# Performance work log

Hardware: AMD Instinct MI355X
Metric: run time of the kernel (lower is better)

The kernel has to match this reference:

```python
import jax, jax.numpy as jnp
import numpy as np

L, B, T, D, H, A, F, V, BIAS_DIM, E = 6, 16, 512, 512, 8, 64, 2048, 10000, 4, 200000
LN_EPS = 1e-3  # keras LayerNormalization default


def positional_encoding(d, max_len):
    pos = np.arange(max_len, dtype=np.float32)[:, None]
    i = np.arange(d, dtype=np.float32)[None, :]
    angle = pos / np.power(10000.0, (2.0 * np.floor(i / 2.0)) / d)
    pe = np.where((np.arange(d) % 2) == 0, np.sin(angle), np.cos(angle))
    return jnp.asarray(pe, jnp.float32)


def layer_norm(x, g, b):
    mu = jnp.mean(x, -1, keepdims=True)
    var = jnp.mean(jnp.square(x - mu), -1, keepdims=True)
    return (x - mu) * jax.lax.rsqrt(var + LN_EPS) * g + b


def attention(x, masks, bias_idx, Wq, Wk, Wv, Wo, be, bs):
    q = jnp.einsum('btd,dha->btha', x, Wq)
    k = jnp.einsum('btd,dha->btha', x, Wk)
    v = jnp.einsum('btd,dha->btha', x, Wv)
    alpha = jnp.einsum('bkha,bqha->bhqk', k, q)
    # sparse edge bias: scalar per edge = bias_embs[type] @ bias_scalar
    ev = (be[bias_idx[:, 0]] @ bs)[:, 0]                      # [E]
    dense = jnp.zeros((x.shape[0], x.shape[1], x.shape[1]), x.dtype)
    dense = dense.at[bias_idx[:, 1], bias_idx[:, 2], bias_idx[:, 3]].add(ev)  # scatter_nd semantics (add)
    ksum = jnp.sum(k, -1)                                     # [B,T,H]
    alpha = alpha + jnp.einsum('bqk,bkh->bhqk', dense, ksum)
    alpha = alpha * jax.lax.rsqrt(jnp.float32(A))
    alpha = alpha * masks + (1.0 - jnp.ceil(masks)) * jnp.finfo(jnp.float32).min
    alpha = jax.nn.softmax(alpha, -1)
    ctx = jnp.einsum('bhqk,bkha->bqha', alpha, v)
    return jnp.einsum('btha,had->btd', ctx, Wo)


def setup_inputs() -> dict:
    key = jax.random.key(0)
    ks = jax.random.split(key, 24)
    tokens = jax.random.randint(ks[0], (B, T), 0, V, dtype=jnp.int32)
    masks = jnp.ones((B, 1, T, T), jnp.float32)
    ab = jnp.stack([
        jax.random.randint(ks[1], (E,), 0, BIAS_DIM, dtype=jnp.int32),
        jax.random.randint(ks[2], (E,), 0, B, dtype=jnp.int32),
        jax.random.randint(ks[3], (E,), 0, T, dtype=jnp.int32),
        jax.random.randint(ks[4], (E,), 0, T, dtype=jnp.int32)], axis=1)
    s = 0.03
    return {
        'tokens': tokens, 'masks': masks, 'attention_bias': ab,
        'embed': jax.random.normal(ks[5], (V, D)) * (D ** -0.5),
        'Wq': jax.random.normal(ks[6], (L, D, H, A)) * s,
        'Wk': jax.random.normal(ks[7], (L, D, H, A)) * s,
        'Wv': jax.random.normal(ks[8], (L, D, H, A)) * s,
        'Wo': jax.random.normal(ks[9], (L, H, A, D)) * s,
        'be': jax.random.normal(ks[10], (L, BIAS_DIM, A)) * s,
        'bs': jax.random.normal(ks[11], (L, A, 1)) * s,
        'ln_g': jnp.ones((L, 2, D)), 'ln_b': jnp.zeros((L, 2, D)),
        'ff1_w': jax.random.normal(ks[12], (L, D, F)) * s,
        'ff1_b': jnp.zeros((L, F)),
        'ff2_w': jax.random.normal(ks[13], (L, F, D)) * s,
        'ff2_b': jnp.zeros((L, D)),
        'lnout_g': jnp.ones((D,)), 'lnout_b': jnp.zeros((D,)),
    }


def reference(tokens, masks, attention_bias, embed, Wq, Wk, Wv, Wo, be, bs,
              ln_g, ln_b, ff1_w, ff1_b, ff2_w, ff2_b, lnout_g, lnout_b):
    pos_enc = positional_encoding(D, 5000)
    x = embed[tokens] * jnp.sqrt(jnp.float32(D)) + pos_enc[:T]
    for l in range(L):
        h = layer_norm(x, ln_g[l, 0], ln_b[l, 0])
        x = x + attention(h, masks, attention_bias, Wq[l], Wk[l], Wv[l], Wo[l], be[l], bs[l])
        h = layer_norm(x, ln_g[l, 1], ln_b[l, 1])
        x = x + jax.nn.relu(h @ ff1_w[l] + ff1_b[l]) @ ff2_w[l] + ff2_b[l]
    return layer_norm(x, lnout_g, lnout_b)
```

## Files before the change

kernel.cpp:

```cpp
#include <hip/hip_runtime.h>
#include <hip/hip_bf16.h>

#define LNUM 6
#define BB 16
#define TT 512
#define DD 512
#define HH 8
#define AA 64
#define FFD 2048
#define EE 200000
#define BIASDIM 4
#define ATT_NEG (-3.402823466e38f)

typedef __bf16 bf16_t;
typedef __attribute__((ext_vector_type(8))) __bf16 bf16x8;
typedef __attribute__((ext_vector_type(4))) float f32x4;

typedef __attribute__((address_space(3))) void lds_void;
typedef const __attribute__((address_space(1))) void glb_void;

__device__ __forceinline__ void async_load16(const bf16_t* g, bf16_t* l) {
    __builtin_amdgcn_global_load_lds((glb_void*)g, (lds_void*)l, 16, 0, 0);
}

__global__ __launch_bounds__(256) void embed_pe_kernel(
    const int* __restrict__ tokens, const float* __restrict__ embed,
    float* __restrict__ x)
{
    int idx = blockIdx.x * 256 + threadIdx.x;
    int d  = idx & (DD - 1);
    int bt = idx >> 9;
    int t  = bt & (TT - 1);
    int tok = tokens[bt];
    float e = embed[(long long)tok * DD + d] * 22.62741699796952f;
    float p = (float)(2 * (d >> 1)) * (1.0f / (float)DD);
    float denom = exp2f(p * 13.287712379549449f);
    float angle = (float)t / denom;
    float pe = (d & 1) ? cosf(angle) : sinf(angle);
    x[idx] = e + pe;
}

template <typename TO>
__global__ __launch_bounds__(256) void ln_kernel(
    const float* __restrict__ x, TO* __restrict__ y,
    const float* __restrict__ g, const float* __restrict__ b)
{
    long long row = blockIdx.x;
    const float* xr = x + row * DD;
    int tid = threadIdx.x;
    float v0 = xr[tid], v1 = xr[tid + 256];
    float s = v0 + v1, sq = v0 * v0 + v1 * v1;
#pragma unroll
    for (int o = 32; o > 0; o >>= 1) {
        s  += __shfl_down(s, o);
        sq += __shfl_down(sq, o);
    }
    __shared__ float ss[4], sq4[4];
    if ((tid & 63) == 0) { ss[tid >> 6] = s; sq4[tid >> 6] = sq; }
    __syncthreads();
    float st  = ss[0] + ss[1] + ss[2] + ss[3];
    float sqt = sq4[0] + sq4[1] + sq4[2] + sq4[3];
    float mean = st * (1.0f / DD);
    float var  = sqt * (1.0f / DD) - mean * mean;
    float inv  = rsqrtf(var + 1e-3f);
    y[row * DD + tid]       = (TO)((v0 - mean) * inv * g[tid]       + b[tid]);
    y[row * DD + tid + 256] = (TO)((v1 - mean) * inv * g[tid + 256] + b[tid + 256]);
}

template <typename TO, int S>
__global__ __launch_bounds__(256) void reduce_ln_kernel(
    float* __restrict__ x, const float* __restrict__ P,
    TO* __restrict__ y, const float* __restrict__ g, const float* __restrict__ b)
{
    const long long NXc = (long long)BB * TT * DD;
    long long row = blockIdx.x;
    int tid = threadIdx.x;
    long long i0 = row * DD + tid;
    float v0 = x[i0], v1 = x[i0 + 256];
#pragma unroll
    for (int s = 0; s < S; s++) {
        v0 += P[(long long)s * NXc + i0];
        v1 += P[(long long)s * NXc + i0 + 256];
    }
    x[i0] = v0; x[i0 + 256] = v1;
    float s2 = v0 + v1, sq = v0 * v0 + v1 * v1;
#pragma unroll
    for (int o = 32; o > 0; o >>= 1) {
        s2 += __shfl_down(s2, o);
        sq += __shfl_down(sq, o);
    }
    __shared__ float ss[4], sq4[4];
    if ((tid & 63) == 0) { ss[tid >> 6] = s2; sq4[tid >> 6] = sq; }
    __syncthreads();
    float st  = ss[0] + ss[1] + ss[2] + ss[3];
    float sqt = sq4[0] + sq4[1] + sq4[2] + sq4[3];
    float mean = st * (1.0f / DD);
    float var  = sqt * (1.0f / DD) - mean * mean;
    float inv  = rsqrtf(var + 1e-3f);
    y[i0]       = (TO)((v0 - mean) * inv * g[tid]       + b[tid]);
    y[i0 + 256] = (TO)((v1 - mean) * inv * g[tid + 256] + b[tid + 256]);
}

__global__ __launch_bounds__(256) void ksum_kernel(
    const bf16_t* __restrict__ k, float* __restrict__ ks)
{
    int idx = blockIdx.x * 256 + threadIdx.x;
    long long base = (long long)idx * AA;
    float s = 0.f;
#pragma unroll
    for (int a = 0; a < AA; a++) s += (float)k[base + a];
    ks[idx] = s;
}

__global__ __launch_bounds__(256) void bias_scatter_kernel(
    const int* __restrict__ ab, const float* __restrict__ be,
    const float* __restrict__ bs, float* __restrict__ dense)
{
    __shared__ float ev[BIASDIM];
    int tid = threadIdx.x;
    if (tid < BIASDIM) {
        float s = 0.f;
        for (int a = 0; a < AA; a++) s += be[tid * AA + a] * bs[a];
        ev[tid] = s;
    }
    __syncthreads();
    int e = blockIdx.x * 256 + tid;
    if (e < EE) {
        int ty = ab[e * 4 + 0];
        int b  = ab[e * 4 + 1];
        int q  = ab[e * 4 + 2];
        int kk = ab[e * 4 + 3];
        unsafeAtomicAdd(&dense[((long long)b * TT + q) * TT + kk], ev[ty]);
    }
}

__global__ __launch_bounds__(256) void wconv_kernel(
    const float* __restrict__ in, bf16_t* __restrict__ out, int R, int Cc)
{
    __shared__ bf16_t tile[64][65];
    int c0 = blockIdx.x * 64, r0 = blockIdx.y * 64;
    int tid = threadIdx.x;
#pragma unroll
    for (int i = 0; i < 16; i++) {
        int idx = tid + i * 256; int r = idx >> 6, c = idx & 63;
        tile[c][r] = (bf16_t)in[(long long)(r0 + r) * Cc + c0 + c];
    }
    __syncthreads();
#pragma unroll
    for (int i = 0; i < 16; i++) {
        int idx = tid + i * 256; int rr = idx >> 6, cc = idx & 63;
        out[(long long)(c0 + rr) * R + r0 + cc] = tile[rr][cc];
    }
}

struct Ptr4 { const float* p[4]; };

__global__ __launch_bounds__(256) void wconv4_kernel(Ptr4 srcs, bf16_t* __restrict__ out)
{
    __shared__ bf16_t tile[64][65];
    int z = blockIdx.z;
    const float* in = srcs.p[z];
    bf16_t* o = out + (long long)z * DD * DD;
    int c0 = blockIdx.x * 64, r0 = blockIdx.y * 64;
    int tid = threadIdx.x;
#pragma unroll
    for (int i = 0; i < 16; i++) {
        int idx = tid + i * 256; int r = idx >> 6, c = idx & 63;
        tile[c][r] = (bf16_t)in[(long long)(r0 + r) * DD + c0 + c];
    }
    __syncthreads();
#pragma unroll
    for (int i = 0; i < 16; i++) {
        int idx = tid + i * 256; int rr = idx >> 6, cc = idx & 63;
        o[(long long)(c0 + rr) * DD + r0 + cc] = tile[rr][cc];
    }
}

__global__ __launch_bounds__(256) void vtrans_kernel(
    const bf16_t* __restrict__ v, bf16_t* __restrict__ vT)
{
    __shared__ bf16_t tile[64][65];
    int bh = blockIdx.y; int b = bh >> 3, h = bh & 7;
    int t0 = blockIdx.x * 64;
    int tid = threadIdx.x;
#pragma unroll
    for (int i = 0; i < 16; i++) {
        int idx = tid + i * 256; int r = idx >> 6, c = idx & 63;
        tile[c][r] = v[((long long)(b * TT + t0 + r) * HH + h) * AA + c];
    }
    __syncthreads();
#pragma unroll
    for (int i = 0; i < 16; i++) {
        int idx = tid + i * 256; int a = idx >> 6, t2 = idx & 63;
        vT[(((long long)b * HH + h) * AA + a) * TT + t0 + t2] = tile[a][t2];
    }
}

__global__ __launch_bounds__(256) void fused_attn_kernel(
    const bf16_t* __restrict__ qg, const bf16_t* __restrict__ kg,
    const bf16_t* __restrict__ vT, const float* __restrict__ dense,
    const float* __restrict__ ksum, const float* __restrict__ masks,
    bf16_t* __restrict__ ctx)
{
    __shared__ __align__(16) bf16_t Ks[64 * 64];
    __shared__ __align__(16) bf16_t Vs[64 * 64];
    __shared__ __align__(16) bf16_t Plds[4 * 16 * 88];

    int tid = threadIdx.x;
    int wave = tid >> 6, lane = tid & 63;
    int row16 = lane & 15, quad = lane >> 4;
    int bh = blockIdx.y; int b = bh >> 3, h = bh & 7;
    int qw = blockIdx.x * 64 + wave * 16;

    bf16x8 qf[2];
    {
        const bf16_t* qp = qg + (((long long)b * TT + qw + row16) * HH + h) * AA + quad * 8;
        qf[0] = *(const bf16x8*)(qp);
        qf[1] = *(const bf16x8*)(qp + 32);
    }

    f32x4 o[4] = {};
    float m_r[4], l_r[4];
#pragma unroll
    for (int r = 0; r < 4; r++) { m_r[r] = -3.0e38f; l_r[r] = 0.f; }

    bf16_t* Pw = Plds + wave * 16 * 88;
    const float* dbase = dense + (long long)b * TT * TT;
    const float* mbase = masks + (long long)b * TT * TT;

    for (int kt = 0; kt < 8; kt++) {
        int t0 = kt * 64;
#pragma unroll
        for (int p = tid; p < 512; p += 256) {
            int r = p >> 3, s = p & 7, c = s ^ (r & 7);
            async_load16(kg + (((long long)b * TT + t0 + r) * HH + h) * AA + c * 8,
                         Ks + p * 8);
        }
#pragma unroll
        for (int p = tid; p < 512; p += 256) {
            int r = p >> 3, s = p & 7, c = s ^ (r & 7);
            async_load16(vT + ((long long)bh * AA + r) * TT + t0 + c * 8,
                         Vs + p * 8);
        }
        __syncthreads();

        f32x4 s4[4] = {};
#pragma unroll
        for (int n = 0; n < 4; n++) {
            int row = n * 16 + row16;
            int sw = row & 7;
            bf16x8 kf0 = *(const bf16x8*)(Ks + row * 64 + ((quad ^ sw) * 8));
            bf16x8 kf1 = *(const bf16x8*)(Ks + row * 64 + (((quad + 4) ^ sw) * 8));
            s4[n] = __builtin_amdgcn_mfma_f32_16x16x32_bf16(qf[0], kf0, s4[n], 0, 0, 0);
            s4[n] = __builtin_amdgcn_mfma_f32_16x16x32_bf16(qf[1], kf1, s4[n], 0, 0, 0);
        }

        float val[4][4];
#pragma unroll
        for (int n = 0; n < 4; n++) {
            int ktok = t0 + n * 16 + row16;
            float ksv = ksum[((long long)b * TT + ktok) * HH + h];
#pragma unroll
            for (int r = 0; r < 4; r++) {
                int qgl = qw + quad * 4 + r;
                float d  = dbase[(long long)qgl * TT + ktok];
                float mk = mbase[(long long)qgl * TT + ktok];
                float vv = 0.125f * fmaf(d, ksv, s4[n][r]);
                val[n][r] = vv * mk + (1.0f - ceilf(mk)) * ATT_NEG;
            }
        }

        float scl[4];
#pragma unroll
        for (int r = 0; r < 4; r++) {
            float mx = fmaxf(fmaxf(val[0][r], val[1][r]), fmaxf(val[2][r], val[3][r]));
#pragma unroll
            for (int off = 1; off < 16; off <<= 1) mx = fmaxf(mx, __shfl_xor(mx, off));
            float mnew = fmaxf(m_r[r], mx);
            float sc = __expf(m_r[r] - mnew);
            float ps = 0.f;
#pragma unroll
            for (int n = 0; n < 4; n++) {
                float p = __expf(val[n][r] - mnew);
                val[n][r] = p;
                ps += p;
            }
#pragma unroll
            for (int off = 1; off < 16; off <<= 1) ps += __shfl_xor(ps, off);
            l_r[r] = l_r[r] * sc + ps;
            m_r[r] = mnew;
            scl[r] = sc;
        }
#pragma unroll
        for (int j = 0; j < 4; j++)
#pragma unroll
            for (int r = 0; r < 4; r++) o[j][r] *= scl[r];

#pragma unroll
        for (int n = 0; n < 4; n++)
#pragma unroll
            for (int r = 0; r < 4; r++)
                Pw[(quad * 4 + r) * 88 + n * 16 + row16] = (bf16_t)val[n][r];
        asm volatile("s_waitcnt lgkmcnt(0)" ::: "memory");

        bf16x8 pa0 = *(const bf16x8*)(Pw + row16 * 88 + quad * 8);
        bf16x8 pa1 = *(const bf16x8*)(Pw + row16 * 88 + 32 + quad * 8);
#pragma unroll
        for (int j = 0; j < 4; j++) {
            int row = j * 16 + row16;
            int sw = row & 7;
            bf16x8 vb0 = *(const bf16x8*)(Vs + row * 64 + ((quad ^ sw) * 8));
            bf16x8 vb1 = *(const bf16x8*)(Vs + row * 64 + (((quad + 4) ^ sw) * 8));
            o[j] = __builtin_amdgcn_mfma_f32_16x16x32_bf16(pa0, vb0, o[j], 0, 0, 0);
            o[j] = __builtin_amdgcn_mfma_f32_16x16x32_bf16(pa1, vb1, o[j], 0, 0, 0);
        }
        __syncthreads();
    }

#pragma unroll
    for (int r = 0; r < 4; r++) {
        float invl = 1.0f / l_r[r];
        int qgl = qw + quad * 4 + r;
        bf16_t* cp = ctx + (((long long)b * TT + qgl) * HH + h) * AA;
#pragma unroll
        for (int j = 0; j < 4; j++)
            cp[j * 16 + row16] = (bf16_t)(o[j][r] * invl);
    }
}

#define PSTAGE(kc0, slot)                                                     \
    {                                                                         \
        bf16_t* At = sm + (slot) * 16384;                                     \
        bf16_t* Bt = At + 8192;                                               \
        _Pragma("unroll")                                                     \
        for (int i = 0; i < 4; i++) {                                         \
            int qq = tid + i * 256;                                           \
            int r = qq >> 3, ck = qq & 7;                                     \
            int cc = (kc0) + ((ck ^ (r & 7)) * 8);                            \
            async_load16(Ag + (long long)(m0 + r) * lda + cc, At + qq * 8);   \
            async_load16(Bg + (long long)(n0 + r) * ldb + cc, Bt + qq * 8);   \
        }                                                                     \
    }

#define PLOAD()                                                               \
    _Pragma("unroll")                                                         \
    for (int mf = 0; mf < 4; mf++) {                                          \
        int ra = wm * 64 + mf * 16 + row16;                                   \
        _Pragma("unroll")                                                     \
        for (int ks2 = 0; ks2 < 2; ks2++)                                     \
            a8[mf][ks2] = *(const bf16x8*)(Ac + ra * 64 +                     \
                              (((ks2 * 4 + quad) ^ (ra & 7)) * 8));           \
    }                                                                         \
    _Pragma("unroll")                                                         \
    for (int nf = 0; nf < 4; nf++) {                                          \
        int rb = wn * 64 + nf * 16 + row16;                                   \
        _Pragma("unroll")                                                     \
        for (int ks2 = 0; ks2 < 2; ks2++)                                     \
            b8[nf][ks2] = *(const bf16x8*)(Bc + rb * 64 +                     \
                              (((ks2 * 4 + quad) ^ (rb & 7)) * 8));           \
    }

#define PMM()                                                                 \
    _Pragma("unroll")                                                         \
    for (int mf = 0; mf < 4; mf++)                                            \
        _Pragma("unroll")                                                     \
        for (int nf = 0; nf < 4; nf++)                                        \
            _Pragma("unroll")                                                 \
            for (int ks2 = 0; ks2 < 2; ks2++)                                 \
                acc[mf][nf] = __builtin_amdgcn_mfma_f32_16x16x32_bf16(        \
                    a8[mf][ks2], b8[nf][ks2], acc[mf][nf], 0, 0, 0);

#define PIPE_BODY(KBEG, NT)                                                   \
    PSTAGE((KBEG), 0);                                                        \
    int c = 0;                                                                \
    for (int t = 0; t < (NT); ++t, c ^= 1) {                                  \
        if (t + 1 < (NT)) {                                                   \
            PSTAGE((KBEG) + (t + 1) * 64, c ^ 1);                             \
            asm volatile("s_waitcnt vmcnt(8)" ::: "memory");                  \
        } else {                                                              \
            asm volatile("s_waitcnt vmcnt(0)" ::: "memory");                  \
        }                                                                     \
        __builtin_amdgcn_sched_barrier(0);                                    \
        __builtin_amdgcn_s_barrier();                                         \
        __builtin_amdgcn_sched_barrier(0);                                    \
        const bf16_t* Ac = sm + c * 16384;                                    \
        const bf16_t* Bc = Ac + 8192;                                         \
        bf16x8 a8[4][2], b8[4][2];                                            \
        PLOAD();                                                              \
        asm volatile("s_waitcnt lgkmcnt(0)" ::: "memory");                    \
        __builtin_amdgcn_sched_barrier(0);                                    \
        __builtin_amdgcn_s_barrier();                                         \
        __builtin_amdgcn_sched_barrier(0);                                    \
        __builtin_amdgcn_s_setprio(1);                                        \
        PMM();                                                                \
        __builtin_amdgcn_s_setprio(0);                                        \
    }

template <typename TC, int ACCUM, int RELU>
__global__ __launch_bounds__(256, 2) void gemm_pipe(
    const bf16_t* __restrict__ Ag, const bf16_t* __restrict__ Bg, TC* __restrict__ Cg,
    int K, int lda, int ldb, int ldc,
    long long sAz, long long sBz, long long sCz,
    const float* __restrict__ bias)
{
    extern __shared__ __align__(16) bf16_t sm[];
    int z = blockIdx.z;
    Ag += z * sAz; Bg += z * sBz; Cg += z * sCz;

    int tid = threadIdx.x;
    int wave = tid >> 6, lane = tid & 63;
    int wm = wave >> 1, wn = wave & 1;
    int row16 = lane & 15, quad = lane >> 4;
    int m0 = blockIdx.x * 128, n0 = blockIdx.y * 128;

    f32x4 acc[4][4] = {};
    int nt = K >> 6;
    PIPE_BODY(0, nt);

#pragma unroll
    for (int mf = 0; mf < 4; mf++) {
#pragma unroll
        for (int nf = 0; nf < 4; nf++) {
#pragma unroll
            for (int r = 0; r < 4; r++) {
                int m = m0 + wm * 64 + mf * 16 + quad * 4 + r;
                int n = n0 + wn * 64 + nf * 16 + row16;
                float vv = acc[mf][nf][r];
                if (bias) vv += bias[n];
                if (ACCUM) vv += (float)Cg[(long long)m * ldc + n];
                if (RELU) vv = fmaxf(vv, 0.f);
                Cg[(long long)m * ldc + n] = (TC)vv;
            }
        }
    }
}

template <int SPLIT>
__global__ __launch_bounds__(256, 2) void gemm_pipe_splitk(
    const bf16_t* __restrict__ Ag, const bf16_t* __restrict__ Bg,
    float* __restrict__ Cg, float* __restrict__ Pg,
    int K, int lda, int ldb, int ldc, const float* __restrict__ bias)
{
    extern __shared__ __align__(16) bf16_t sm[];
    int z = blockIdx.z;
    int kbeg = z * (K / SPLIT);

    int tid = threadIdx.x;
    int wave = tid >> 6, lane = tid & 63;
    int wm = wave >> 1, wn = wave & 1;
    int row16 = lane & 15, quad = lane >> 4;
    int m0 = blockIdx.x * 128, n0 = blockIdx.y * 128;

    f32x4 acc[4][4] = {};
    int nt = (K / SPLIT) >> 6;
    PIPE_BODY(kbeg, nt);

    const long long NXc = (long long)BB * TT * DD;
#pragma unroll
    for (int mf = 0; mf < 4; mf++) {
#pragma unroll
        for (int nf = 0; nf < 4; nf++) {
#pragma unroll
            for (int r = 0; r < 4; r++) {
                int m = m0 + wm * 64 + mf * 16 + quad * 4 + r;
                int n = n0 + wn * 64 + nf * 16 + row16;
                float vv = acc[mf][nf][r];
                long long ci = (long long)m * ldc + n;
                if (z == 0) {
                    if (bias) vv += bias[n];
                    Cg[ci] = Cg[ci] + vv;
                } else {
                    Pg[(long long)(z - 1) * NXc + ci] = vv;
                }
            }
        }
    }
}

extern "C" void kernel_launch(void* const* d_in, const int* in_sizes, int n_in,
                              void* d_out, int out_size, void* d_ws, size_t ws_size,
                              hipStream_t stream)
{
    const int*   tokens = (const int*)d_in[0];
    const float* masks  = (const float*)d_in[1];
    const int*   ab     = (const int*)d_in[2];
    const float* embed  = (const float*)d_in[3];
    const float* Wq     = (const float*)d_in[4];
    const float* Wk     = (const float*)d_in[5];
    const float* Wv     = (const float*)d_in[6];
    const float* Wo     = (const float*)d_in[7];
    const float* be     = (const float*)d_in[8];
    const float* bs     = (const float*)d_in[9];
    const float* ln_g   = (const float*)d_in[10];
    const float* ln_b   = (const float*)d_in[11];
    const float* ff1w   = (const float*)d_in[12];
    const float* ff1b   = (const float*)d_in[13];
    const float* ff2w   = (const float*)d_in[14];
    const float* ff2b   = (const float*)d_in[15];
    const float* lng    = (const float*)d_in[16];
    const float* lnb    = (const float*)d_in[17];
    float* out = (float*)d_out;

    const long long NX = (long long)BB * TT * DD;
    float* x     = (float*)d_ws;
    float* ks    = x + NX;
    bf16_t* h_bf = (bf16_t*)(ks + (long long)BB * TT * HH);
    float* dense = (float*)(h_bf + NX);
    bf16_t* q    = (bf16_t*)(dense + (long long)BB * TT * TT);
    bf16_t* k    = q + NX;
    bf16_t* v    = k + NX;
    bf16_t* vT   = v + NX;
    bf16_t* wqT  = vT + NX;
    bf16_t* wkT  = wqT + (long long)DD * DD;
    bf16_t* wvT  = wkT + (long long)DD * DD;
    bf16_t* woT  = wvT + (long long)DD * DD;
    bf16_t* ff1T = woT + (long long)DD * DD;
    bf16_t* ff2T = ff1T + (long long)DD * FFD;
    bf16_t* ffm  = ff2T + (long long)FFD * DD;

    float* partCtx = dense;
    float* partFF  = dense;

    const size_t LDSP = 65536;

    embed_pe_kernel<<<dim3(NX / 256), dim3(256), 0, stream>>>(tokens, embed, x);

    for (int l = 0; l < LNUM; l++) {
        if (l == 0) {
            ln_kernel<bf16_t><<<dim3(BB * TT), dim3(256), 0, stream>>>(
                x, h_bf, ln_g + (l * 2 + 0) * DD, ln_b + (l * 2 + 0) * DD);
        } else {
            reduce_ln_kernel<bf16_t, 3><<<dim3(BB * TT), dim3(256), 0, stream>>>(
                x, partFF, h_bf, ln_g + (l * 2 + 0) * DD, ln_b + (l * 2 + 0) * DD);
        }

        Ptr4 p4;
        p4.p[0] = Wq + (long long)l * DD * HH * AA;
        p4.p[1] = Wk + (long long)l * DD * HH * AA;
        p4.p[2] = Wv + (long long)l * DD * HH * AA;
        p4.p[3] = Wo + (long long)l * HH * AA * DD;
        wconv4_kernel<<<dim3(8, 8, 4), dim3(256), 0, stream>>>(p4, wqT);
        wconv_kernel<<<dim3(FFD / 64, DD / 64, 1), dim3(256), 0, stream>>>(
            ff1w + (long long)l * DD * FFD, ff1T, DD, FFD);
        wconv_kernel<<<dim3(DD / 64, FFD / 64, 1), dim3(256), 0, stream>>>(
            ff2w + (long long)l * FFD * DD, ff2T, FFD, DD);

        const float* ff1b_l = ff1b + (long long)l * FFD;
        const float* ff2b_l = ff2b + (long long)l * DD;

        gemm_pipe<bf16_t, 0, 0><<<dim3(64, 4, 3), dim3(256), LDSP, stream>>>(
            h_bf, wqT, q, 512, 512, 512, 512,
            0LL, (long long)DD * DD, NX, nullptr);

        vtrans_kernel<<<dim3(8, BB * HH), dim3(256), 0, stream>>>(v, vT);
        ksum_kernel<<<dim3(BB * TT * HH / 256), dim3(256), 0, stream>>>(k, ks);

        hipMemsetAsync(dense, 0, sizeof(float) * (size_t)BB * TT * TT, stream);
        bias_scatter_kernel<<<dim3((EE + 255) / 256), dim3(256), 0, stream>>>(
            ab, be + (long long)l * BIASDIM * AA, bs + (long long)l * AA, dense);

        fused_attn_kernel<<<dim3(TT / 64, BB * HH), dim3(256), 0, stream>>>(
            q, k, vT, dense, ks, masks, h_bf);

        gemm_pipe_splitk<2><<<dim3(64, 4, 2), dim3(256), LDSP, stream>>>(
            h_bf, woT, x, partCtx, 512, 512, 512, 512, nullptr);

        reduce_ln_kernel<bf16_t, 1><<<dim3(BB * TT), dim3(256), 0, stream>>>(
            x, partCtx, h_bf, ln_g + (l * 2 + 1) * DD, ln_b + (l * 2 + 1) * DD);

        gemm_pipe<bf16_t, 0, 1><<<dim3(64, 16, 1), dim3(256), LDSP, stream>>>(
            h_bf, ff1T, ffm, 512, 512, 512, 2048, 0LL, 0LL, 0LL, ff1b_l);

        gemm_pipe_splitk<4><<<dim3(64, 4, 4), dim3(256), LDSP, stream>>>(
            ffm, ff2T, x, partFF, 2048, 2048, 2048, 512, ff2b_l);
    }

    reduce_ln_kernel<float, 3><<<dim3(BB * TT), dim3(256), 0, stream>>>(
        x, partFF, out, lng, lnb);
}
```

Before: 1.532 ms.

## Pack bias and mask into bf16 pairs, prefetch them, set MFMA priority, reduce FF2 split-K

```diff
diff --git a/kernel.cpp b/kernel.cpp
--- a/kernel.cpp
+++ b/kernel.cpp
@@ -134,6 +134,20 @@
     }
 }
 
+__global__ __launch_bounds__(256) void pack_dm_kernel(
+    float* __restrict__ dense, const float* __restrict__ masks)
+{
+    long long i = ((long long)blockIdx.x * 256 + threadIdx.x) * 4;
+    f32x4 d = *(const f32x4*)(dense + i);
+    f32x4 m = *(const f32x4*)(masks + i);
+    unsigned int w[4];
+#pragma unroll
+    for (int j = 0; j < 4; j++)
+        w[j] = (__float_as_uint(m[j]) & 0xffff0000u) |
+               (__float_as_uint(d[j]) >> 16);
+    *(uint4*)(dense + i) = *(const uint4*)w;
+}
+
 __global__ __launch_bounds__(256) void wconv_kernel(
     const float* __restrict__ in, bf16_t* __restrict__ out, int R, int Cc)
 {
@@ -198,9 +212,8 @@
 
 __global__ __launch_bounds__(256) void fused_attn_kernel(
     const bf16_t* __restrict__ qg, const bf16_t* __restrict__ kg,
-    const bf16_t* __restrict__ vT, const float* __restrict__ dense,
-    const float* __restrict__ ksum, const float* __restrict__ masks,
-    bf16_t* __restrict__ ctx)
+    const bf16_t* __restrict__ vT, const unsigned int* __restrict__ dm,
+    const float* __restrict__ ksum, bf16_t* __restrict__ ctx)
 {
     __shared__ __align__(16) bf16_t Ks[64 * 64];
     __shared__ __align__(16) bf16_t Vs[64 * 64];
@@ -225,11 +238,23 @@
     for (int r = 0; r < 4; r++) { m_r[r] = -3.0e38f; l_r[r] = 0.f; }
 
     bf16_t* Pw = Plds + wave * 16 * 88;
-    const float* dbase = dense + (long long)b * TT * TT;
-    const float* mbase = masks + (long long)b * TT * TT;
+    const unsigned int* dmbase = dm + (long long)b * TT * TT;
+    const float* ksbase = ksum + (long long)b * TT * HH + h;
 
     for (int kt = 0; kt < 8; kt++) {
         int t0 = kt * 64;
+
+        unsigned int dmw[4][4];
+        float ksv4[4];
+#pragma unroll
+        for (int n = 0; n < 4; n++) {
+            int ktok = t0 + n * 16 + row16;
+            ksv4[n] = ksbase[(long long)ktok * HH];
+#pragma unroll
+            for (int r = 0; r < 4; r++)
+                dmw[n][r] = dmbase[(long long)(qw + quad * 4 + r) * TT + ktok];
+        }
+
 #pragma unroll
         for (int p = tid; p < 512; p += 256) {
             int r = p >> 3, s = p & 7, c = s ^ (r & 7);
@@ -245,6 +270,7 @@
         __syncthreads();
 
         f32x4 s4[4] = {};
+        __builtin_amdgcn_s_setprio(1);
 #pragma unroll
         for (int n = 0; n < 4; n++) {
             int row = n * 16 + row16;
@@ -254,19 +280,18 @@
             s4[n] = __builtin_amdgcn_mfma_f32_16x16x32_bf16(qf[0], kf0, s4[n], 0, 0, 0);
             s4[n] = __builtin_amdgcn_mfma_f32_16x16x32_bf16(qf[1], kf1, s4[n], 0, 0, 0);
         }
+        __builtin_amdgcn_s_setprio(0);
 
         float val[4][4];
 #pragma unroll
         for (int n = 0; n < 4; n++) {
-            int ktok = t0 + n * 16 + row16;
-            float ksv = ksum[((long long)b * TT + ktok) * HH + h];
 #pragma unroll
             for (int r = 0; r < 4; r++) {
-                int qgl = qw + quad * 4 + r;
-                float d  = dbase[(long long)qgl * TT + ktok];
-                float mk = mbase[(long long)qgl * TT + ktok];
-                float vv = 0.125f * fmaf(d, ksv, s4[n][r]);
-                val[n][r] = vv * mk + (1.0f - ceilf(mk)) * ATT_NEG;
+                unsigned int w = dmw[n][r];
+                float d  = __uint_as_float(w << 16);
+                float mk = __uint_as_float(w & 0xffff0000u);
+                float vv = 0.125f * fmaf(d, ksv4[n], s4[n][r]);
+                val[n][r] = (mk == 0.f) ? -3.0e38f : vv * mk;
             }
         }
 
@@ -305,6 +330,7 @@
 
         bf16x8 pa0 = *(const bf16x8*)(Pw + row16 * 88 + quad * 8);
         bf16x8 pa1 = *(const bf16x8*)(Pw + row16 * 88 + 32 + quad * 8);
+        __builtin_amdgcn_s_setprio(1);
 #pragma unroll
         for (int j = 0; j < 4; j++) {
             int row = j * 16 + row16;
@@ -314,6 +340,7 @@
             o[j] = __builtin_amdgcn_mfma_f32_16x16x32_bf16(pa0, vb0, o[j], 0, 0, 0);
             o[j] = __builtin_amdgcn_mfma_f32_16x16x32_bf16(pa1, vb1, o[j], 0, 0, 0);
         }
+        __builtin_amdgcn_s_setprio(0);
         __syncthreads();
     }
 
@@ -530,7 +557,7 @@
             ln_kernel<bf16_t><<<dim3(BB * TT), dim3(256), 0, stream>>>(
                 x, h_bf, ln_g + (l * 2 + 0) * DD, ln_b + (l * 2 + 0) * DD);
         } else {
-            reduce_ln_kernel<bf16_t, 3><<<dim3(BB * TT), dim3(256), 0, stream>>>(
+            reduce_ln_kernel<bf16_t, 1><<<dim3(BB * TT), dim3(256), 0, stream>>>(
                 x, partFF, h_bf, ln_g + (l * 2 + 0) * DD, ln_b + (l * 2 + 0) * DD);
         }
 
@@ -558,9 +585,11 @@
         hipMemsetAsync(dense, 0, sizeof(float) * (size_t)BB * TT * TT, stream);
         bias_scatter_kernel<<<dim3((EE + 255) / 256), dim3(256), 0, stream>>>(
             ab, be + (long long)l * BIASDIM * AA, bs + (long long)l * AA, dense);
+        pack_dm_kernel<<<dim3((int)(BB * TT * TT / 1024)), dim3(256), 0, stream>>>(
+            dense, masks);
 
         fused_attn_kernel<<<dim3(TT / 64, BB * HH), dim3(256), 0, stream>>>(
-            q, k, vT, dense, ks, masks, h_bf);
+            q, k, vT, (const unsigned int*)dense, ks, h_bf);
 
         gemm_pipe_splitk<2><<<dim3(64, 4, 2), dim3(256), LDSP, stream>>>(
             h_bf, woT, x, partCtx, 512, 512, 512, 512, nullptr);
@@ -571,10 +600,10 @@
         gemm_pipe<bf16_t, 0, 1><<<dim3(64, 16, 1), dim3(256), LDSP, stream>>>(
             h_bf, ff1T, ffm, 512, 512, 512, 2048, 0LL, 0LL, 0LL, ff1b_l);
 
-        gemm_pipe_splitk<4><<<dim3(64, 4, 4), dim3(256), LDSP, stream>>>(
+        gemm_pipe_splitk<2><<<dim3(64, 4, 2), dim3(256), LDSP, stream>>>(
             ffm, ff2T, x, partFF, 2048, 2048, 2048, 512, ff2b_l);
     }
 
-    reduce_ln_kernel<float, 3><<<dim3(BB * TT), dim3(256), 0, stream>>>(
+    reduce_ln_kernel<float, 1><<<dim3(BB * TT), dim3(256), 0, stream>>>(
         x, partFF, out, lng, lnb);
 }
```

After: 1.613 ms. 1.05x slower.
